# Optimization experiments

Measured on AMD Instinct MI355X. Metric: run time of the kernel, lower is better.

The kernel has to match this reference:

```python
import jax, jax.numpy as jnp
import numpy as np

B, C, NZ, NY, NX = 4, 64, 1, 496, 432
N_PER = 16000  # pillars per sample


def setup_inputs() -> dict:
    key = jax.random.key(0)
    rng = np.random.default_rng(0)
    coords_list = []
    for b in range(B):
        # unique (y, x) cells per sample so scatter writes never collide
        flat = rng.choice(NY * NX, size=N_PER, replace=False).astype(np.int64)
        y, x = flat // NX, flat % NX
        z = np.zeros(N_PER, np.int64)  # nz == 1 -> z coordinate is always 0
        bb = np.full(N_PER, b, np.int64)
        coords_list.append(np.stack([bb, z, y, x], axis=1))
    coords = jnp.asarray(np.concatenate(coords_list, axis=0))  # [N, 4]
    voxel_features = jax.random.normal(key, (B * N_PER, C), dtype=jnp.float32)
    return {
        "voxel_features": voxel_features,
        "coords": coords,
        "batch_size": B,
        "nz": NZ,
        "ny": NY,
        "nx": NX,
    }


def reference(voxel_features, coords, batch_size, nz, ny, nx):
    # Faithful to torch: per-sample index = y*nz + z*nx + x into a canvas of
    # length nz*ny*nx (note the original's unusual index formula; with nz=1,
    # z=0 this is y*nx + x). We fuse all batches into one scatter using a
    # batch-aware flat index.
    spatial = nz * ny * nx
    c = voxel_features.shape[1]
    flat_idx = (coords[:, 0] * spatial
                + coords[:, 1] * nz
                + coords[:, 2] * nx
                + coords[:, 3])  # [N]
    canvas = jnp.zeros((batch_size * spatial, c), dtype=voxel_features.dtype)
    canvas = canvas.at[flat_idx].set(voxel_features)  # single fused scatter
    # [B, spatial, C] -> [B, C, spatial] -> [B, C*nz, ny, nx]
    canvas = canvas.reshape(batch_size, spatial, c).transpose(0, 2, 1)
    return canvas.reshape(batch_size, c * nz, ny, nx)
```

## Files before the change

### kernel.cpp

```cpp
#include <hip/hip_runtime.h>


__global__ void pps_build_idx(const int* __restrict__ coords,
                              const int* __restrict__ nz_p,
                              const int* __restrict__ ny_p,
                              const int* __restrict__ nx_p,
                              int* __restrict__ idxmap, int n_points) {
    int n = blockIdx.x * blockDim.x + threadIdx.x;
    if (n >= n_points) return;
    int nz = nz_p[0], ny = ny_p[0], nx = nx_p[0];
    long long spatial = (long long)nz * ny * nx;
    int b = coords[4 * n + 0];
    int z = coords[4 * n + 1];
    int y = coords[4 * n + 2];
    int x = coords[4 * n + 3];
    long long cell = b * spatial + (long long)z * nz + (long long)y * nx + x;
    idxmap[cell] = n;
}

__global__ __launch_bounds__(256)
void pps_gather_v5(const float* __restrict__ vf,
                   const int* __restrict__ idxmap,
                   const int* __restrict__ nz_p,
                   const int* __restrict__ ny_p,
                   const int* __restrict__ nx_p,
                   float* __restrict__ out,
                   int C, long long ncells) {
    const int spatial =
        __builtin_amdgcn_readfirstlane(nz_p[0] * ny_p[0] * nx_p[0]);
    const long long nquads = (ncells + 3) >> 2;
    long long q = blockIdx.x * (long long)blockDim.x + threadIdx.x;
    if (q >= nquads) return;

    long long cell = q << 2;
    unsigned int ucell = (unsigned int)cell;
    unsigned int b = ucell / (unsigned int)spatial;
    unsigned int s = ucell - b * (unsigned int)spatial;

    if (cell + 3 < ncells && s + 3 < (unsigned int)spatial && (C & 3) == 0) {
        int4 iv = *reinterpret_cast<const int4*>(idxmap + cell);
        const bool vx = iv.x >= 0, vy = iv.y >= 0, vz = iv.z >= 0, vw = iv.w >= 0;
        const float* px = vf + (long long)iv.x * C;
        const float* py = vf + (long long)iv.y * C;
        const float* pz = vf + (long long)iv.z * C;
        const float* pw = vf + (long long)iv.w * C;
        float* op0 = out + ((long long)b * C) * spatial + s;

        #pragma unroll 4
        for (int cc = 0; cc < C; cc += 4) {
            float4 rx = make_float4(0.f, 0.f, 0.f, 0.f);
            float4 ry = rx, rz = rx, rw = rx;
            if (vx) rx = *reinterpret_cast<const float4*>(px + cc);
            if (vy) ry = *reinterpret_cast<const float4*>(py + cc);
            if (vz) rz = *reinterpret_cast<const float4*>(pz + cc);
            if (vw) rw = *reinterpret_cast<const float4*>(pw + cc);
            float* op = op0 + (long long)cc * spatial;
            *reinterpret_cast<float4*>(op) = make_float4(rx.x, ry.x, rz.x, rw.x);
            op += spatial;
            *reinterpret_cast<float4*>(op) = make_float4(rx.y, ry.y, rz.y, rw.y);
            op += spatial;
            *reinterpret_cast<float4*>(op) = make_float4(rx.z, ry.z, rz.z, rw.z);
            op += spatial;
            *reinterpret_cast<float4*>(op) = make_float4(rx.w, ry.w, rz.w, rw.w);
        }
    } else {
        for (int j = 0; j < 4; ++j) {
            long long cc = cell + j;
            if (cc >= ncells) break;
            long long bb = cc / spatial;
            long long ss = cc - bb * spatial;
            int idx = idxmap[cc];
            for (int c = 0; c < C; ++c)
                out[(bb * C + c) * spatial + ss] =
                    (idx >= 0) ? vf[(long long)idx * C + c] : 0.0f;
        }
    }
}

__global__ void pps_scatter_kernel(const float* __restrict__ vf,
                                   const int* __restrict__ coords,
                                   const int* __restrict__ nz_p,
                                   const int* __restrict__ ny_p,
                                   const int* __restrict__ nx_p,
                                   float* __restrict__ out,
                                   int n_points, int C) {
    int idx = blockIdx.x * blockDim.x + threadIdx.x;
    int total = n_points * C;
    if (idx >= total) return;
    int n = idx / C;
    int c = idx - n * C;
    int nz = nz_p[0], ny = ny_p[0], nx = nx_p[0];
    long long spatial = (long long)nz * ny * nx;
    int b = coords[4 * n + 0];
    int z = coords[4 * n + 1];
    int y = coords[4 * n + 2];
    int x = coords[4 * n + 3];
    long long s = (long long)z * nz + (long long)y * nx + (long long)x;
    out[((long long)b * C + c) * spatial + s] = vf[idx];
}

extern "C" void kernel_launch(void* const* d_in, const int* in_sizes, int n_in,
                              void* d_out, int out_size, void* d_ws, size_t ws_size,
                              hipStream_t stream) {
    const float* vf     = (const float*)d_in[0];
    const int*   coords = (const int*)d_in[1];
    const int*   nz_p   = (const int*)d_in[3];
    const int*   ny_p   = (const int*)d_in[4];
    const int*   nx_p   = (const int*)d_in[5];
    float* out = (float*)d_out;

    int n_points = in_sizes[1] / 4;
    int C        = in_sizes[0] / n_points;
    long long ncells = (long long)out_size / C;
    size_t idx_bytes = (size_t)ncells * sizeof(int);

    if (ws_size >= idx_bytes && ncells < 0x7FFFFFFFLL) {
        int* idxmap = (int*)d_ws;
        (void)hipMemsetAsync(idxmap, 0xFF, idx_bytes, stream);
        {
            int block = 256;
            int grid = (n_points + block - 1) / block;
            pps_build_idx<<<grid, block, 0, stream>>>(coords, nz_p, ny_p, nx_p,
                                                      idxmap, n_points);
        }
        {
            int block = 256;
            long long nquads = (ncells + 3) / 4;
            long long gx = (nquads + block - 1) / block;
            if (gx > 0x7FFFFFFF) gx = 0x7FFFFFFF;
            pps_gather_v5<<<(int)gx, block, 0, stream>>>(vf, idxmap, nz_p, ny_p,
                                                         nx_p, out, C, ncells);
        }
    } else {
        (void)hipMemsetAsync(d_out, 0, (size_t)out_size * sizeof(float), stream);
        int total = n_points * C;
        int block = 256;
        int grid  = (total + block - 1) / block;
        pps_scatter_kernel<<<grid, block, 0, stream>>>(vf, coords, nz_p, ny_p,
                                                       nx_p, out, n_points, C);
    }
}
```

Before: 47.83 us.

## Stage occupied pillar rows in LDS with coalesced loads before transposed writes

Adds a C=64 gather kernel in which each block first compacts its non-empty cells into LDS slots with a shared atomic counter. It then loads the referenced feature rows with coalesced 16-thread float4 reads into a padded LDS buffer, and reads them back from LDS for the transposed output stores. This replaces the scattered per-thread 256-byte row reads of the old kernel with cooperative loads. In exchange it adds LDS atomics, two block barriers and about 52KB of shared memory per block, which may reduce occupancy. It falls back to direct global reads when a block has more than 192 occupied cells.

```diff
diff --git a/kernel.cpp b/kernel.cpp
--- a/kernel.cpp
+++ b/kernel.cpp
@@ -1,5 +1,8 @@
 #include <hip/hip_runtime.h>
 
+
+#define PPS_MAXSLOTS 192
+#define PPS_ROWSTRIDE 68
 
 __global__ void pps_build_idx(const int* __restrict__ coords,
                               const int* __restrict__ nz_p,
@@ -19,6 +22,119 @@
 }
 
 __global__ __launch_bounds__(256)
+void pps_gather_v6(const float* __restrict__ vf,
+                   const int* __restrict__ idxmap,
+                   const int* __restrict__ nz_p,
+                   const int* __restrict__ ny_p,
+                   const int* __restrict__ nx_p,
+                   float* __restrict__ out,
+                   long long ncells) {
+    __shared__ float rows[(PPS_MAXSLOTS + 1) * PPS_ROWSTRIDE];
+    __shared__ int slots_idx[PPS_MAXSLOTS + 1];
+    __shared__ int cnt;
+
+    const int spatial =
+        __builtin_amdgcn_readfirstlane(nz_p[0] * ny_p[0] * nx_p[0]);
+    const int t = threadIdx.x;
+    if (t == 0) cnt = 0;
+    __syncthreads();
+
+    long long q = blockIdx.x * 256LL + t;
+    long long cell = q << 2;
+    const bool in_range = (cell + 3 < ncells);
+
+    int4 iv = make_int4(-1, -1, -1, -1);
+    int sx = 0, sy = 0, sz = 0, sw = 0;
+    unsigned int b = 0, s = 0;
+    if (in_range) {
+        unsigned int ucell = (unsigned int)cell;
+        b = ucell / (unsigned int)spatial;
+        s = ucell - b * (unsigned int)spatial;
+        iv = *reinterpret_cast<const int4*>(idxmap + cell);
+        if (iv.x >= 0) { int sl = atomicAdd(&cnt, 1);
+            if (sl < PPS_MAXSLOTS) { sx = sl + 1; slots_idx[sl + 1] = iv.x; } else sx = -1; }
+        if (iv.y >= 0) { int sl = atomicAdd(&cnt, 1);
+            if (sl < PPS_MAXSLOTS) { sy = sl + 1; slots_idx[sl + 1] = iv.y; } else sy = -1; }
+        if (iv.z >= 0) { int sl = atomicAdd(&cnt, 1);
+            if (sl < PPS_MAXSLOTS) { sz = sl + 1; slots_idx[sl + 1] = iv.z; } else sz = -1; }
+        if (iv.w >= 0) { int sl = atomicAdd(&cnt, 1);
+            if (sl < PPS_MAXSLOTS) { sw = sl + 1; slots_idx[sl + 1] = iv.w; } else sw = -1; }
+    }
+    __syncthreads();
+
+    const int total = cnt;
+    const int nv = total < PPS_MAXSLOTS ? total : PPS_MAXSLOTS;
+    const int part = t & 15;
+    if (t < 16) {
+        float4 zero = make_float4(0.f, 0.f, 0.f, 0.f);
+        *reinterpret_cast<float4*>(&rows[part * 4]) = zero;
+    }
+    for (int slot = 1 + (t >> 4); slot <= nv; slot += 16) {
+        int src = slots_idx[slot];
+        float4 v = *reinterpret_cast<const float4*>(vf + src * 64 + part * 4);
+        *reinterpret_cast<float4*>(&rows[slot * PPS_ROWSTRIDE + part * 4]) = v;
+    }
+    __syncthreads();
+
+    if (!in_range) {
+        for (int j = 0; j < 4; ++j) {
+            long long cc = cell + j;
+            if (cc < 0 || cc >= ncells) continue;
+            long long bb = cc / spatial;
+            long long ss = cc - bb * spatial;
+            int idx = idxmap[cc];
+            for (int c = 0; c < 64; ++c)
+                out[(bb * 64 + c) * (long long)spatial + ss] =
+                    (idx >= 0) ? vf[(long long)idx * 64 + c] : 0.0f;
+        }
+        return;
+    }
+
+    float* op0 = out + ((long long)b * 64) * spatial + s;
+
+    if (total <= PPS_MAXSLOTS) {
+        #pragma unroll 4
+        for (int cc = 0; cc < 64; cc += 4) {
+            float4 rx = *reinterpret_cast<const float4*>(&rows[sx * PPS_ROWSTRIDE + cc]);
+            float4 ry = *reinterpret_cast<const float4*>(&rows[sy * PPS_ROWSTRIDE + cc]);
+            float4 rz = *reinterpret_cast<const float4*>(&rows[sz * PPS_ROWSTRIDE + cc]);
+            float4 rw = *reinterpret_cast<const float4*>(&rows[sw * PPS_ROWSTRIDE + cc]);
+            float* op = op0 + (long long)cc * spatial;
+            *reinterpret_cast<float4*>(op) = make_float4(rx.x, ry.x, rz.x, rw.x);
+            op += spatial;
+            *reinterpret_cast<float4*>(op) = make_float4(rx.y, ry.y, rz.y, rw.y);
+            op += spatial;
+            *reinterpret_cast<float4*>(op) = make_float4(rx.z, ry.z, rz.z, rw.z);
+            op += spatial;
+            *reinterpret_cast<float4*>(op) = make_float4(rx.w, ry.w, rz.w, rw.w);
+        }
+    } else {
+        const bool vx = iv.x >= 0, vy = iv.y >= 0, vz = iv.z >= 0, vw = iv.w >= 0;
+        const float* px = vf + (long long)iv.x * 64;
+        const float* py = vf + (long long)iv.y * 64;
+        const float* pz = vf + (long long)iv.z * 64;
+        const float* pw = vf + (long long)iv.w * 64;
+        #pragma unroll 4
+        for (int cc = 0; cc < 64; cc += 4) {
+            float4 rx = make_float4(0.f, 0.f, 0.f, 0.f);
+            float4 ry = rx, rz = rx, rw = rx;
+            if (vx) rx = *reinterpret_cast<const float4*>(px + cc);
+            if (vy) ry = *reinterpret_cast<const float4*>(py + cc);
+            if (vz) rz = *reinterpret_cast<const float4*>(pz + cc);
+            if (vw) rw = *reinterpret_cast<const float4*>(pw + cc);
+            float* op = op0 + (long long)cc * spatial;
+            *reinterpret_cast<float4*>(op) = make_float4(rx.x, ry.x, rz.x, rw.x);
+            op += spatial;
+            *reinterpret_cast<float4*>(op) = make_float4(rx.y, ry.y, rz.y, rw.y);
+            op += spatial;
+            *reinterpret_cast<float4*>(op) = make_float4(rx.z, ry.z, rz.z, rw.z);
+            op += spatial;
+            *reinterpret_cast<float4*>(op) = make_float4(rx.w, ry.w, rz.w, rw.w);
+        }
+    }
+}
+
+__global__ __launch_bounds__(256)
 void pps_gather_v5(const float* __restrict__ vf,
                    const int* __restrict__ idxmap,
                    const int* __restrict__ nz_p,
@@ -31,7 +147,6 @@
     const long long nquads = (ncells + 3) >> 2;
     long long q = blockIdx.x * (long long)blockDim.x + threadIdx.x;
     if (q >= nquads) return;
-
     long long cell = q << 2;
     unsigned int ucell = (unsigned int)cell;
     unsigned int b = ucell / (unsigned int)spatial;
@@ -45,7 +160,6 @@
         const float* pz = vf + (long long)iv.z * C;
         const float* pw = vf + (long long)iv.w * C;
         float* op0 = out + ((long long)b * C) * spatial + s;
-
         #pragma unroll 4
         for (int cc = 0; cc < C; cc += 4) {
             float4 rx = make_float4(0.f, 0.f, 0.f, 0.f);
@@ -71,7 +185,7 @@
             long long ss = cc - bb * spatial;
             int idx = idxmap[cc];
             for (int c = 0; c < C; ++c)
-                out[(bb * C + c) * spatial + ss] =
+                out[(bb * C + c) * (long long)spatial + ss] =
                     (idx >= 0) ? vf[(long long)idx * C + c] : 0.0f;
         }
     }
@@ -123,13 +237,17 @@
             pps_build_idx<<<grid, block, 0, stream>>>(coords, nz_p, ny_p, nx_p,
                                                       idxmap, n_points);
         }
-        {
-            int block = 256;
-            long long nquads = (ncells + 3) / 4;
-            long long gx = (nquads + block - 1) / block;
+        long long nquads = (ncells + 3) / 4;
+        if (C == 64 && (ncells & 3) == 0) {
+            long long gx = (nquads + 255) / 256;
             if (gx > 0x7FFFFFFF) gx = 0x7FFFFFFF;
-            pps_gather_v5<<<(int)gx, block, 0, stream>>>(vf, idxmap, nz_p, ny_p,
-                                                         nx_p, out, C, ncells);
+            pps_gather_v6<<<(int)gx, 256, 0, stream>>>(vf, idxmap, nz_p, ny_p,
+                                                       nx_p, out, ncells);
+        } else {
+            long long gx = (nquads + 255) / 256;
+            if (gx > 0x7FFFFFFF) gx = 0x7FFFFFFF;
+            pps_gather_v5<<<(int)gx, 256, 0, stream>>>(vf, idxmap, nz_p, ny_p,
+                                                       nx_p, out, C, ncells);
         }
     } else {
         (void)hipMemsetAsync(d_out, 0, (size_t)out_size * sizeof(float), stream);
```

Result: no change. 47.69 us (-0.3%).
